# Optimization experiments

Measured on AMD Instinct MI355X. Metric: run time of the kernel, lower is better.

## Reference

```python
import jax, jax.numpy as jnp
import numpy as np

N, K = 50000, 16          # nodes, fixed neighbor-list length
IN, HID, OUT = 11, 64, 1  # temporal feat dim, hidden, output


def setup_inputs() -> dict:
    key = jax.random.key(0)
    ks = iter(jax.random.split(key, 64))
    def rn(shape, scale=1.0):
        return jax.random.normal(next(ks), shape, dtype=jnp.float32) * scale
    inp = {
        "x": rn((N, IN)),
        "neighbors": jax.random.randint(next(ks), (N, K), 0, N, dtype=jnp.int32),
        "prev_hidden": rn((N, HID)),
    }
    # DGL SAGEConv(lstm): LSTM(in=d, hid=d), fc_self Linear(d,o,bias=True), fc_neigh Linear(d,o,bias=False)
    dims = [(IN, HID), (HID, HID), (HID, HID), (HID, OUT)]
    for li, (d, o) in enumerate(dims, start=1):
        s = 1.0 / np.sqrt(d)
        inp[f"l{li}_Wih"] = rn((4 * d, d), s)
        inp[f"l{li}_Whh"] = rn((4 * d, d), s)
        inp[f"l{li}_bih"] = rn((4 * d,), s)
        inp[f"l{li}_bhh"] = rn((4 * d,), s)
        inp[f"l{li}_Ws"] = rn((o, d), s)
        inp[f"l{li}_bs"] = rn((o,), s)
        inp[f"l{li}_Wn"] = rn((o, d), s)
    sg = 1.0 / np.sqrt(HID)
    inp["g_Wih"] = rn((3 * HID, HID), sg)
    inp["g_Whh"] = rn((3 * HID, HID), sg)
    inp["g_bih"] = rn((3 * HID,), sg)
    inp["g_bhh"] = rn((3 * HID,), sg)
    return inp


def _sage_conv(h, neighbors, Wih, Whh, bih, bhh, Ws, bs, Wn):
    """DGL SAGEConv with aggregator_type='lstm'."""
    m = h[neighbors]             # [N, K, D] gathered neighbor messages
    ms = jnp.swapaxes(m, 0, 1)   # [K, N, D] time-major for scan
    Nn, D = h.shape
    h0 = jnp.zeros((Nn, D), h.dtype)

    def step(carry, mt):
        hp, cp = carry
        g = mt @ Wih.T + bih + hp @ Whh.T + bhh   # [N, 4D]
        i, f, gg, o = jnp.split(g, 4, axis=-1)    # torch LSTM gate order i,f,g,o
        c = jax.nn.sigmoid(f) * cp + jax.nn.sigmoid(i) * jnp.tanh(gg)
        hn = jax.nn.sigmoid(o) * jnp.tanh(c)
        return (hn, c), None

    (hK, _), _ = jax.lax.scan(step, (h0, h0), ms)  # final hidden state = neighbor agg
    return h @ Ws.T + bs + hK @ Wn.T


def _gru(x, h, Wih, Whh, bih, bhh):
    """torch.nn.GRUCell, gate order r,z,n."""
    gi = x @ Wih.T + bih
    gh = h @ Whh.T + bhh
    ir, iz, inn = jnp.split(gi, 3, axis=-1)
    hr, hz, hn = jnp.split(gh, 3, axis=-1)
    r = jax.nn.sigmoid(ir + hr)
    z = jax.nn.sigmoid(iz + hz)
    n = jnp.tanh(inn + r * hn)
    return (1.0 - z) * n + z * h


def reference(x, neighbors, prev_hidden,
              l1_Wih, l1_Whh, l1_bih, l1_bhh, l1_Ws, l1_bs, l1_Wn,
              l2_Wih, l2_Whh, l2_bih, l2_bhh, l2_Ws, l2_bs, l2_Wn,
              l3_Wih, l3_Whh, l3_bih, l3_bhh, l3_Ws, l3_bs, l3_Wn,
              l4_Wih, l4_Whh, l4_bih, l4_bhh, l4_Ws, l4_bs, l4_Wn,
              g_Wih, g_Whh, g_bih, g_bhh):
    h = jax.nn.relu(_sage_conv(x, neighbors, l1_Wih, l1_Whh, l1_bih, l1_bhh, l1_Ws, l1_bs, l1_Wn))
    h = jax.nn.relu(_sage_conv(h, neighbors, l2_Wih, l2_Whh, l2_bih, l2_bhh, l2_Ws, l2_bs, l2_Wn))
    h = jax.nn.relu(_sage_conv(h, neighbors, l3_Wih, l3_Whh, l3_bih, l3_bhh, l3_Ws, l3_bs, l3_Wn))
    h = _gru(h, prev_hidden, g_Wih, g_Whh, g_bih, g_bhh)
    logits = _sage_conv(h, neighbors, l4_Wih, l4_Whh, l4_bih, l4_bhh, l4_Ws, l4_bs, l4_Wn)
    return logits
```

## Files before the change

kernel.cpp:

```cpp
#include <hip/hip_runtime.h>

#define N_NODES 50000

typedef __bf16 bf16x8 __attribute__((ext_vector_type(8)));
typedef float f32x4 __attribute__((ext_vector_type(4)));

union U16x8 { uint4 v; unsigned short u[8]; bf16x8 b; };

__device__ __forceinline__ float b2f(unsigned short h){
  unsigned int u = ((unsigned int)h) << 16;
  return __builtin_bit_cast(float, u);
}
__device__ __forceinline__ unsigned short f2b(float x){
  unsigned int u = __builtin_bit_cast(unsigned int, x);
  u = u + 0x7FFFu + ((u >> 16) & 1u);
  return (unsigned short)(u >> 16);
}
__device__ __forceinline__ float sigm(float x){
  const float e = __builtin_amdgcn_exp2f(x * -1.4426950408889634f);
  return __builtin_amdgcn_rcpf(1.0f + e);
}
__device__ __forceinline__ float tanh_(float x){
  const float e = __builtin_amdgcn_exp2f(x * 2.8853900817779268f);
  return fmaf(-2.0f, __builtin_amdgcn_rcpf(1.0f + e), 1.0f);
}

__device__ __forceinline__ bf16x8 load8_bf16(const float* p){
  float4 a = *(const float4*)p; float4 c = *(const float4*)(p + 4);
  U16x8 r;
  r.u[0]=f2b(a.x); r.u[1]=f2b(a.y); r.u[2]=f2b(a.z); r.u[3]=f2b(a.w);
  r.u[4]=f2b(c.x); r.u[5]=f2b(c.y); r.u[6]=f2b(c.z); r.u[7]=f2b(c.w);
  return r.b;
}


__global__ __launch_bounds__(256) void l1_kernel(
    const float* __restrict__ x, const int* __restrict__ nbr,
    const float* __restrict__ Wih, const float* __restrict__ Whh,
    const float* __restrict__ bih, const float* __restrict__ bhh,
    const float* __restrict__ Ws,  const float* __restrict__ bs,
    const float* __restrict__ Wn,  unsigned short* __restrict__ out_hl)
{
  __shared__ unsigned short mbuf[16][16][24];
  __shared__ unsigned short hbuf[2][16][24];

  const int tid  = threadIdx.x;
  const int wave = tid >> 6, lane = tid & 63;
  const int n16  = lane & 15, q = lane >> 4;
  const int nb0  = blockIdx.x * 16;

  { unsigned int* p = (unsigned int*)hbuf;
    for (int i = tid; i < 384; i += 256) p[i] = 0u; }

  {
    const int nd = tid >> 4, t = tid & 15;
    const int gn = nbr[(nb0 + nd) * 16 + t];
    const float* row = x + (long)gn * 11;
    float v[16];
    #pragma unroll
    for (int j = 0; j < 11; j++) v[j] = row[j];
    #pragma unroll
    for (int j = 11; j < 16; j++) v[j] = 0.f;
    U16x8 A, B;
    #pragma unroll
    for (int j = 0; j < 8; j++){ A.u[j] = f2b(v[j]); B.u[j] = f2b(v[8 + j]); }
    *(uint4*)&mbuf[t][nd][0] = A.v;
    *(uint4*)&mbuf[t][nd][8] = B.v;
  }

  bf16x8 wf[4];
  float bg4[4];
  #pragma unroll
  for (int g = 0; g < 4; g++){
    const int u = n16;
    const float* src = (q < 2) ? (Wih + (g * 11 + u) * 11)
                               : (Whh + (g * 11 + u) * 11);
    const int kb = (q & 1) * 8;
    U16x8 a;
    #pragma unroll
    for (int j = 0; j < 8; j++){
      const int k = kb + j;
      float v = (u < 11 && k < 11) ? src[k] : 0.f;
      a.u[j] = f2b(v);
    }
    wf[g] = a.b;
    bg4[g] = (n16 < 11) ? (bih[g * 11 + n16] + bhh[g * 11 + n16]) : 0.f;
  }

  float c_ = 0.f;
  __syncthreads();

  for (int t = 0; t < 16; t++){
    const int db = t & 1, nb = db ^ 1;

    const unsigned short* ph = (q < 2) ? &mbuf[t][n16][q * 8]
                                       : &hbuf[db][n16][(q - 2) * 8];
    U16x8 ah; ah.v = *(const uint4*)ph;

    f32x4 acc[4];
    #pragma unroll
    for (int g = 0; g < 4; g++){
      f32x4 av = {bg4[g], bg4[g], bg4[g], bg4[g]};
      acc[g] = __builtin_amdgcn_mfma_f32_16x16x32_bf16(ah.b, wf[g], av, 0, 0, 0);
    }

    {
      const float iv = sigm(acc[0][wave]);
      const float fv = sigm(acc[1][wave]);
      const float gg = tanh_(acc[2][wave]);
      const float ov = sigm(acc[3][wave]);
      c_ = fv * c_ + iv * gg;
      hbuf[nb][q * 4 + wave][n16] = f2b(ov * tanh_(c_));
    }
    __syncthreads();
  }

  U16x8 ea;
  if (q < 2){
    const float* row = x + (long)(nb0 + n16) * 11;
    U16x8 H;
    #pragma unroll
    for (int j = 0; j < 8; j++){
      const int k = q * 8 + j;
      H.u[j] = f2b((k < 11) ? row[k] : 0.f);
    }
    ea = H;
  } else {
    ea.v = *(const uint4*)&hbuf[0][n16][(q - 2) * 8];
  }

  bf16x8 ewf;
  {
    const int uo = wave * 16 + n16;
    const float* src = (q < 2) ? (Ws + uo * 11) : (Wn + uo * 11);
    const int kb = (q & 1) * 8;
    U16x8 a;
    #pragma unroll
    for (int j = 0; j < 8; j++){
      const int k = kb + j;
      a.u[j] = f2b((k < 11) ? src[k] : 0.f);
    }
    ewf = a.b;
  }

  {
    const int uo = wave * 16 + n16;
    const float bsv = bs[uo];
    f32x4 e = {bsv, bsv, bsv, bsv};
    e = __builtin_amdgcn_mfma_f32_16x16x32_bf16(ea.b, ewf, e, 0, 0, 0);
    #pragma unroll
    for (int r = 0; r < 4; r++)
      out_hl[(size_t)(nb0 + q * 4 + r) * 64 + uo] = f2b(fmaxf(e[r], 0.f));
  }
}

__global__ __launch_bounds__(256, 3) void sage64_kernel(
    const unsigned short* __restrict__ in_hl, const int* __restrict__ nbr,
    const float* __restrict__ Wih, const float* __restrict__ Whh,
    const float* __restrict__ bih, const float* __restrict__ bhh,
    const float* __restrict__ Ws,  const float* __restrict__ bs,
    const float* __restrict__ Wn,
    unsigned short* __restrict__ out_hl, float* __restrict__ out_f32, int mode)
{
  __shared__ uint4 mbuf[8][16][8];
  __shared__ uint4 hbuf[2][16][8];

  const int tid = threadIdx.x;
  const int wv = tid >> 6, lane = tid & 63;
  const int n16 = lane & 15, q = lane >> 4;
  const int nb0 = blockIdx.x * 16;

  auto refill = [&](int base){
    const int nd = tid >> 4, sub = tid & 15;
    const int tr = sub >> 1, half = sub & 1;
    const int t_ = base + tr;
    const int gn = nbr[(nb0 + nd) * 16 + t_];
    const uint4* src = (const uint4*)(in_hl + (size_t)gn * 64);
    #pragma unroll
    for (int j = 0; j < 4; j++){
      const int s = half * 4 + j;
      mbuf[tr][nd][(s + nd + t_) & 7] = src[s];
    }
  };

  refill(0);
  { unsigned int* p = (unsigned int*)&hbuf[0][0][0];
    for (int i = tid; i < 512; i += 256) p[i] = 0u; }

  bf16x8 wih_f[4][2], whh_f[4][2];
  #pragma unroll
  for (int g = 0; g < 4; g++){
    const int row = g * 64 + wv * 16 + n16;
    #pragma unroll
    for (int kc = 0; kc < 2; kc++){
      wih_f[g][kc] = load8_bf16(Wih + row * 64 + kc * 32 + q * 8);
      whh_f[g][kc] = load8_bf16(Whh + row * 64 + kc * 32 + q * 8);
    }
  }
  f32x4 bg[4];
  #pragma unroll
  for (int g = 0; g < 4; g++){
    float4 bi = *(const float4*)(bih + g * 64 + wv * 16 + q * 4);
    float4 bh = *(const float4*)(bhh + g * 64 + wv * 16 + q * 4);
    f32x4 s = {bi.x + bh.x, bi.y + bh.y, bi.z + bh.z, bi.w + bh.w};
    bg[g] = s;
  }

  float c4[4] = {0.f, 0.f, 0.f, 0.f};
  __syncthreads();

  for (int t = 0; t < 16; t++){
    if (t == 8){
      refill(8);
      __syncthreads();
    }
    const int db = t & 1, nbf = db ^ 1;

    bf16x8 mh[2], hh[2];
    #pragma unroll
    for (int kc = 0; kc < 2; kc++){
      U16x8 a; a.v = mbuf[t & 7][n16][(kc * 4 + q + n16 + t) & 7]; mh[kc] = a.b;
      U16x8 c_; c_.v = hbuf[db][n16][(kc * 4 + q + n16) & 7];      hh[kc] = c_.b;
    }

    f32x4 acc[4];
    #pragma unroll
    for (int g = 0; g < 4; g++) acc[g] = bg[g];
    #pragma unroll
    for (int kc = 0; kc < 2; kc++){
      #pragma unroll
      for (int g = 0; g < 4; g++)
        acc[g] = __builtin_amdgcn_mfma_f32_16x16x32_bf16(wih_f[g][kc], mh[kc], acc[g], 0, 0, 0);
      #pragma unroll
      for (int g = 0; g < 4; g++)
        acc[g] = __builtin_amdgcn_mfma_f32_16x16x32_bf16(whh_f[g][kc], hh[kc], acc[g], 0, 0, 0);
    }

    unsigned short hB[4];
    #pragma unroll
    for (int r = 0; r < 4; r++){
      const float iv = sigm(acc[0][r]);
      const float fv = sigm(acc[1][r]);
      const float gg = tanh_(acc[2][r]);
      const float ov = sigm(acc[3][r]);
      c4[r] = fv * c4[r] + iv * gg;
      hB[r] = f2b(ov * tanh_(c4[r]));
    }
    {
      const int idx = wv * 4 + q;
      const int slot = idx >> 1, half = idx & 1;
      ((uint2*)&hbuf[nbf][n16][(slot + n16) & 7])[half] =
          make_uint2((unsigned)hB[0] | ((unsigned)hB[1] << 16),
                     (unsigned)hB[2] | ((unsigned)hB[3] << 16));
    }
    __syncthreads();
  }

  bf16x8 sH[2], kH[2];
  #pragma unroll
  for (int kc = 0; kc < 2; kc++){
    U16x8 a; a.v = *(const uint4*)(in_hl + (size_t)(nb0 + n16) * 64 + kc * 32 + q * 8);
    sH[kc] = a.b;
    U16x8 c_; c_.v = hbuf[0][n16][(kc * 4 + q + n16) & 7]; kH[kc] = c_.b;
  }

  if (mode == 0){
    bf16x8 ws_f[2], wn_f[2];
    #pragma unroll
    for (int kc = 0; kc < 2; kc++){
      ws_f[kc] = load8_bf16(Ws + (wv * 16 + n16) * 64 + kc * 32 + q * 8);
      wn_f[kc] = load8_bf16(Wn + (wv * 16 + n16) * 64 + kc * 32 + q * 8);
    }
    float4 bsv = *(const float4*)(bs + wv * 16 + q * 4);
    f32x4 e = {bsv.x, bsv.y, bsv.z, bsv.w};
    #pragma unroll
    for (int kc = 0; kc < 2; kc++){
      e = __builtin_amdgcn_mfma_f32_16x16x32_bf16(ws_f[kc], sH[kc], e, 0, 0, 0);
      e = __builtin_amdgcn_mfma_f32_16x16x32_bf16(wn_f[kc], kH[kc], e, 0, 0, 0);
    }
    unsigned short oB[4];
    #pragma unroll
    for (int r = 0; r < 4; r++) oB[r] = f2b(fmaxf(e[r], 0.f));
    *(uint2*)(out_hl + (size_t)(nb0 + n16) * 64 + wv * 16 + q * 4) =
        make_uint2((unsigned)oB[0] | ((unsigned)oB[1] << 16),
                   (unsigned)oB[2] | ((unsigned)oB[3] << 16));
  } else {
    if (wv == 0){
      bf16x8 ws_f[2], wn_f[2];
      #pragma unroll
      for (int kc = 0; kc < 2; kc++){
        U16x8 a, b_;
        a.v = make_uint4(0u,0u,0u,0u); b_.v = make_uint4(0u,0u,0u,0u);
        if (n16 == 0){
          a.b  = load8_bf16(Ws + kc * 32 + q * 8);
          b_.b = load8_bf16(Wn + kc * 32 + q * 8);
        }
        ws_f[kc] = a.b; wn_f[kc] = b_.b;
      }
      f32x4 e = {0.f, 0.f, 0.f, 0.f};
      #pragma unroll
      for (int kc = 0; kc < 2; kc++){
        e = __builtin_amdgcn_mfma_f32_16x16x32_bf16(ws_f[kc], sH[kc], e, 0, 0, 0);
        e = __builtin_amdgcn_mfma_f32_16x16x32_bf16(wn_f[kc], kH[kc], e, 0, 0, 0);
      }
      if (q == 0) out_f32[nb0 + n16] = e[0] + bs[0];
    }
  }
}

__global__ __launch_bounds__(256) void gru_kernel(
    const unsigned short* __restrict__ h3_hl, const float* __restrict__ prev,
    const float* __restrict__ gWih, const float* __restrict__ gWhh,
    const float* __restrict__ gbih, const float* __restrict__ gbhh,
    unsigned short* __restrict__ out_hl)
{
  const int tid = threadIdx.x, wave = tid >> 6, lane = tid & 63;
  const int n16 = lane & 15, q = lane >> 4;
  const int nb0 = blockIdx.x * 16;
  const int u_ = wave * 16 + n16;

  bf16x8 ah[2], ap[2];
  #pragma unroll
  for (int kc = 0; kc < 2; kc++){
    U16x8 a; a.v = *(const uint4*)(h3_hl + (size_t)(nb0 + n16) * 64 + kc * 32 + q * 8);
    ah[kc] = a.b;
    ap[kc] = load8_bf16(prev + (size_t)(nb0 + n16) * 64 + kc * 32 + q * 8);
  }

  bf16x8 wi_f[3][2], wh_f[3][2];
  #pragma unroll
  for (int g = 0; g < 3; g++){
    const int row = g * 64 + wave * 16 + n16;
    #pragma unroll
    for (int kc = 0; kc < 2; kc++){
      wi_f[g][kc] = load8_bf16(gWih + row * 64 + kc * 32 + q * 8);
      wh_f[g][kc] = load8_bf16(gWhh + row * 64 + kc * 32 + q * 8);
    }
  }

  f32x4 gi[3], gh[3];
  #pragma unroll
  for (int g = 0; g < 3; g++){
    const float bi = gbih[g * 64 + u_], bh = gbhh[g * 64 + u_];
    f32x4 vi = {bi, bi, bi, bi}; gi[g] = vi;
    f32x4 vh = {bh, bh, bh, bh}; gh[g] = vh;
  }
  #pragma unroll
  for (int kc = 0; kc < 2; kc++){
    #pragma unroll
    for (int g = 0; g < 3; g++)
      gi[g] = __builtin_amdgcn_mfma_f32_16x16x32_bf16(ah[kc], wi_f[g][kc], gi[g], 0, 0, 0);
    #pragma unroll
    for (int g = 0; g < 3; g++)
      gh[g] = __builtin_amdgcn_mfma_f32_16x16x32_bf16(ap[kc], wh_f[g][kc], gh[g], 0, 0, 0);
  }

  #pragma unroll
  for (int r = 0; r < 4; r++){
    const long node = nb0 + q * 4 + r;
    const float rv = sigm(gi[0][r] + gh[0][r]);
    const float zv = sigm(gi[1][r] + gh[1][r]);
    const float nv = tanh_(gi[2][r] + rv * gh[2][r]);
    const float hp = prev[node * 64 + u_];
    const float v = (1.f - zv) * nv + zv * hp;
    out_hl[(size_t)node * 64 + u_] = f2b(v);
  }
}

extern "C" void kernel_launch(void* const* d_in, const int* in_sizes, int n_in,
                              void* d_out, int out_size, void* d_ws, size_t ws_size,
                              hipStream_t stream)
{
  (void)in_sizes; (void)n_in; (void)out_size; (void)ws_size;
  const float* x    = (const float*)d_in[0];
  const int*   nbr  = (const int*)d_in[1];
  const float* prev = (const float*)d_in[2];
  auto W = [&](int i){ return (const float*)d_in[i]; };

  unsigned short* tabA = (unsigned short*)d_ws;
  unsigned short* tabB = tabA + (size_t)N_NODES * 64;

  l1_kernel<<<N_NODES / 16, 256, 0, stream>>>(
      x, nbr, W(3), W(4), W(5), W(6), W(7), W(8), W(9), tabA);
  sage64_kernel<<<N_NODES / 16, 256, 0, stream>>>(
      tabA, nbr, W(10), W(11), W(12), W(13), W(14), W(15), W(16), tabB, nullptr, 0);
  sage64_kernel<<<N_NODES / 16, 256, 0, stream>>>(
      tabB, nbr, W(17), W(18), W(19), W(20), W(21), W(22), W(23), tabA, nullptr, 0);
  gru_kernel<<<N_NODES / 16, 256, 0, stream>>>(
      tabA, prev, W(31), W(32), W(33), W(34), tabB);
  sage64_kernel<<<N_NODES / 16, 256, 0, stream>>>(
      tabB, nbr, W(24), W(25), W(26), W(27), W(28), W(29), W(30),
      nullptr, (float*)d_out, 1);
}
```

Measured before the change: 532.8 us.

## Process two 16-node groups per block in sage64 LSTM kernel

Each sage64 block now handles 32 nodes as two independent 16-node groups. Per-wave weight fragments in registers and the per-step barriers are shared across both groups, and the interleaved MFMA chains of the two groups give independent work to hide MFMA latency. In exchange the kernel uses twice the LDS and more registers, which may lower occupancy under the existing launch bounds, and the grid is halved, with guards for a partial last block.

```diff
diff --git a/kernel.cpp b/kernel.cpp
--- a/kernel.cpp
+++ b/kernel.cpp
@@ -162,30 +162,35 @@
     const float* __restrict__ Wn,
     unsigned short* __restrict__ out_hl, float* __restrict__ out_f32, int mode)
 {
-  __shared__ uint4 mbuf[8][16][8];
-  __shared__ uint4 hbuf[2][16][8];
+  __shared__ uint4 mbuf[2][8][16][8];
+  __shared__ uint4 hbuf[2][2][16][8];
 
   const int tid = threadIdx.x;
   const int wv = tid >> 6, lane = tid & 63;
   const int n16 = lane & 15, q = lane >> 4;
-  const int nb0 = blockIdx.x * 16;
-
-  auto refill = [&](int base){
+  const int nb0 = blockIdx.x * 32;
+  const int nb1 = nb0 + 16;
+  const bool v1 = (nb1 < N_NODES);
+
+  auto refill = [&](int grp, int base){
     const int nd = tid >> 4, sub = tid & 15;
     const int tr = sub >> 1, half = sub & 1;
     const int t_ = base + tr;
-    const int gn = nbr[(nb0 + nd) * 16 + t_];
+    int node = (grp ? nb1 : nb0) + nd;
+    if (node >= N_NODES) node = 0;
+    const int gn = nbr[node * 16 + t_];
     const uint4* src = (const uint4*)(in_hl + (size_t)gn * 64);
     #pragma unroll
     for (int j = 0; j < 4; j++){
       const int s = half * 4 + j;
-      mbuf[tr][nd][(s + nd + t_) & 7] = src[s];
+      mbuf[grp][tr][nd][(s + nd + t_) & 7] = src[s];
     }
   };
 
-  refill(0);
-  { unsigned int* p = (unsigned int*)&hbuf[0][0][0];
-    for (int i = tid; i < 512; i += 256) p[i] = 0u; }
+  refill(0, 0);
+  refill(1, 0);
+  { unsigned int* p = (unsigned int*)hbuf;
+    for (int i = tid; i < 2048; i += 256) p[i] = 0u; }
 
   bf16x8 wih_f[4][2], whh_f[4][2];
   #pragma unroll
@@ -206,62 +211,78 @@
     bg[g] = s;
   }
 
-  float c4[4] = {0.f, 0.f, 0.f, 0.f};
+  float c4[2][4] = {{0.f,0.f,0.f,0.f},{0.f,0.f,0.f,0.f}};
   __syncthreads();
 
   for (int t = 0; t < 16; t++){
     if (t == 8){
-      refill(8);
+      refill(0, 8);
+      refill(1, 8);
       __syncthreads();
     }
     const int db = t & 1, nbf = db ^ 1;
 
-    bf16x8 mh[2], hh[2];
+    bf16x8 mh[2][2], hh[2][2];
+    #pragma unroll
+    for (int grp = 0; grp < 2; grp++){
+      #pragma unroll
+      for (int kc = 0; kc < 2; kc++){
+        U16x8 a; a.v = mbuf[grp][t & 7][n16][(kc * 4 + q + n16 + t) & 7]; mh[grp][kc] = a.b;
+        U16x8 c_; c_.v = hbuf[grp][db][n16][(kc * 4 + q + n16) & 7];      hh[grp][kc] = c_.b;
+      }
+    }
+
+    f32x4 acc[2][4];
+    #pragma unroll
+    for (int grp = 0; grp < 2; grp++)
+      #pragma unroll
+      for (int g = 0; g < 4; g++) acc[grp][g] = bg[g];
     #pragma unroll
     for (int kc = 0; kc < 2; kc++){
-      U16x8 a; a.v = mbuf[t & 7][n16][(kc * 4 + q + n16 + t) & 7]; mh[kc] = a.b;
-      U16x8 c_; c_.v = hbuf[db][n16][(kc * 4 + q + n16) & 7];      hh[kc] = c_.b;
-    }
-
-    f32x4 acc[4];
-    #pragma unroll
-    for (int g = 0; g < 4; g++) acc[g] = bg[g];
-    #pragma unroll
-    for (int kc = 0; kc < 2; kc++){
-      #pragma unroll
-      for (int g = 0; g < 4; g++)
-        acc[g] = __builtin_amdgcn_mfma_f32_16x16x32_bf16(wih_f[g][kc], mh[kc], acc[g], 0, 0, 0);
-      #pragma unroll
-      for (int g = 0; g < 4; g++)
-        acc[g] = __builtin_amdgcn_mfma_f32_16x16x32_bf16(whh_f[g][kc], hh[kc], acc[g], 0, 0, 0);
-    }
-
-    unsigned short hB[4];
-    #pragma unroll
-    for (int r = 0; r < 4; r++){
-      const float iv = sigm(acc[0][r]);
-      const float fv = sigm(acc[1][r]);
-      const float gg = tanh_(acc[2][r]);
-      const float ov = sigm(acc[3][r]);
-      c4[r] = fv * c4[r] + iv * gg;
-      hB[r] = f2b(ov * tanh_(c4[r]));
-    }
-    {
+      #pragma unroll
+      for (int g = 0; g < 4; g++){
+        acc[0][g] = __builtin_amdgcn_mfma_f32_16x16x32_bf16(wih_f[g][kc], mh[0][kc], acc[0][g], 0, 0, 0);
+        acc[1][g] = __builtin_amdgcn_mfma_f32_16x16x32_bf16(wih_f[g][kc], mh[1][kc], acc[1][g], 0, 0, 0);
+      }
+      #pragma unroll
+      for (int g = 0; g < 4; g++){
+        acc[0][g] = __builtin_amdgcn_mfma_f32_16x16x32_bf16(whh_f[g][kc], hh[0][kc], acc[0][g], 0, 0, 0);
+        acc[1][g] = __builtin_amdgcn_mfma_f32_16x16x32_bf16(whh_f[g][kc], hh[1][kc], acc[1][g], 0, 0, 0);
+      }
+    }
+
+    #pragma unroll
+    for (int grp = 0; grp < 2; grp++){
+      unsigned short hB[4];
+      #pragma unroll
+      for (int r = 0; r < 4; r++){
+        const float iv = sigm(acc[grp][0][r]);
+        const float fv = sigm(acc[grp][1][r]);
+        const float gg = tanh_(acc[grp][2][r]);
+        const float ov = sigm(acc[grp][3][r]);
+        c4[grp][r] = fv * c4[grp][r] + iv * gg;
+        hB[r] = f2b(ov * tanh_(c4[grp][r]));
+      }
       const int idx = wv * 4 + q;
       const int slot = idx >> 1, half = idx & 1;
-      ((uint2*)&hbuf[nbf][n16][(slot + n16) & 7])[half] =
+      ((uint2*)&hbuf[grp][nbf][n16][(slot + n16) & 7])[half] =
           make_uint2((unsigned)hB[0] | ((unsigned)hB[1] << 16),
                      (unsigned)hB[2] | ((unsigned)hB[3] << 16));
     }
     __syncthreads();
   }
 
-  bf16x8 sH[2], kH[2];
-  #pragma unroll
-  for (int kc = 0; kc < 2; kc++){
-    U16x8 a; a.v = *(const uint4*)(in_hl + (size_t)(nb0 + n16) * 64 + kc * 32 + q * 8);
-    sH[kc] = a.b;
-    U16x8 c_; c_.v = hbuf[0][n16][(kc * 4 + q + n16) & 7]; kH[kc] = c_.b;
+  bf16x8 sH[2][2], kH[2][2];
+  #pragma unroll
+  for (int grp = 0; grp < 2; grp++){
+    int node = (grp ? nb1 : nb0) + n16;
+    if (node >= N_NODES) node = 0;
+    #pragma unroll
+    for (int kc = 0; kc < 2; kc++){
+      U16x8 a; a.v = *(const uint4*)(in_hl + (size_t)node * 64 + kc * 32 + q * 8);
+      sH[grp][kc] = a.b;
+      U16x8 c_; c_.v = hbuf[grp][0][n16][(kc * 4 + q + n16) & 7]; kH[grp][kc] = c_.b;
+    }
   }
 
   if (mode == 0){
@@ -272,20 +293,25 @@
       wn_f[kc] = load8_bf16(Wn + (wv * 16 + n16) * 64 + kc * 32 + q * 8);
     }
     float4 bsv = *(const float4*)(bs + wv * 16 + q * 4);
-    f32x4 e = {bsv.x, bsv.y, bsv.z, bsv.w};
-    #pragma unroll
-    for (int kc = 0; kc < 2; kc++){
-      e = __builtin_amdgcn_mfma_f32_16x16x32_bf16(ws_f[kc], sH[kc], e, 0, 0, 0);
-      e = __builtin_amdgcn_mfma_f32_16x16x32_bf16(wn_f[kc], kH[kc], e, 0, 0, 0);
-    }
-    unsigned short oB[4];
-    #pragma unroll
-    for (int r = 0; r < 4; r++) oB[r] = f2b(fmaxf(e[r], 0.f));
-    *(uint2*)(out_hl + (size_t)(nb0 + n16) * 64 + wv * 16 + q * 4) =
-        make_uint2((unsigned)oB[0] | ((unsigned)oB[1] << 16),
-                   (unsigned)oB[2] | ((unsigned)oB[3] << 16));
+    #pragma unroll
+    for (int grp = 0; grp < 2; grp++){
+      if (grp == 1 && !v1) break;
+      f32x4 e = {bsv.x, bsv.y, bsv.z, bsv.w};
+      #pragma unroll
+      for (int kc = 0; kc < 2; kc++){
+        e = __builtin_amdgcn_mfma_f32_16x16x32_bf16(ws_f[kc], sH[grp][kc], e, 0, 0, 0);
+        e = __builtin_amdgcn_mfma_f32_16x16x32_bf16(wn_f[kc], kH[grp][kc], e, 0, 0, 0);
+      }
+      unsigned short oB[4];
+      #pragma unroll
+      for (int r = 0; r < 4; r++) oB[r] = f2b(fmaxf(e[r], 0.f));
+      *(uint2*)(out_hl + (size_t)((grp ? nb1 : nb0) + n16) * 64 + wv * 16 + q * 4) =
+          make_uint2((unsigned)oB[0] | ((unsigned)oB[1] << 16),
+                     (unsigned)oB[2] | ((unsigned)oB[3] << 16));
+    }
   } else {
-    if (wv == 0){
+    if (wv < 2 && !(wv == 1 && !v1)){
+      const int grp = wv;
       bf16x8 ws_f[2], wn_f[2];
       #pragma unroll
       for (int kc = 0; kc < 2; kc++){
@@ -300,10 +326,10 @@
       f32x4 e = {0.f, 0.f, 0.f, 0.f};
       #pragma unroll
       for (int kc = 0; kc < 2; kc++){
-        e = __builtin_amdgcn_mfma_f32_16x16x32_bf16(ws_f[kc], sH[kc], e, 0, 0, 0);
-        e = __builtin_amdgcn_mfma_f32_16x16x32_bf16(wn_f[kc], kH[kc], e, 0, 0, 0);
-      }
-      if (q == 0) out_f32[nb0 + n16] = e[0] + bs[0];
+        e = __builtin_amdgcn_mfma_f32_16x16x32_bf16(ws_f[kc], sH[grp][kc], e, 0, 0, 0);
+        e = __builtin_amdgcn_mfma_f32_16x16x32_bf16(wn_f[kc], kH[grp][kc], e, 0, 0, 0);
+      }
+      if (q == 0) out_f32[(grp ? nb1 : nb0) + n16] = e[0] + bs[0];
     }
   }
 }
@@ -380,15 +406,17 @@
   unsigned short* tabA = (unsigned short*)d_ws;
   unsigned short* tabB = tabA + (size_t)N_NODES * 64;
 
+  const int sage_grid = (N_NODES + 31) / 32;
+
   l1_kernel<<<N_NODES / 16, 256, 0, stream>>>(
       x, nbr, W(3), W(4), W(5), W(6), W(7), W(8), W(9), tabA);
-  sage64_kernel<<<N_NODES / 16, 256, 0, stream>>>(
+  sage64_kernel<<<sage_grid, 256, 0, stream>>>(
       tabA, nbr, W(10), W(11), W(12), W(13), W(14), W(15), W(16), tabB, nullptr, 0);
-  sage64_kernel<<<N_NODES / 16, 256, 0, stream>>>(
+  sage64_kernel<<<sage_grid, 256, 0, stream>>>(
       tabB, nbr, W(17), W(18), W(19), W(20), W(21), W(22), W(23), tabA, nullptr, 0);
   gru_kernel<<<N_NODES / 16, 256, 0, stream>>>(
       tabA, prev, W(31), W(32), W(33), W(34), tabB);
-  sage64_kernel<<<N_NODES / 16, 256, 0, stream>>>(
+  sage64_kernel<<<sage_grid, 256, 0, stream>>>(
       tabB, nbr, W(24), W(25), W(26), W(27), W(28), W(29), W(30),
       nullptr, (float*)d_out, 1);
 }
```

After: 547.8 us. 1.03x slower.

## Fuse GRU cell into layer-3 SAGE kernel and prefetch all 16 neighbor steps

Applied to the files above, without the earlier changes.

The GRU cell now runs in the epilogue of the third SAGE layer: the layer-3 output tile goes into shared memory and the GRU matmuls are done in the same block. This drops a kernel launch and one global write and read of the intermediate activations. Separately, the neighbor-message buffer is doubled so all 16 timesteps are gathered up front, which removes the mid-loop refill and its barrier. The price is double the shared memory for mbuf (32KB) and more register pressure, which may reduce occupancy under launch_bounds(256,3).

```diff
diff --git a/kernel.cpp b/kernel.cpp
--- a/kernel.cpp
+++ b/kernel.cpp
@@ -160,9 +160,12 @@
     const float* __restrict__ bih, const float* __restrict__ bhh,
     const float* __restrict__ Ws,  const float* __restrict__ bs,
     const float* __restrict__ Wn,
+    const float* __restrict__ gWih, const float* __restrict__ gWhh,
+    const float* __restrict__ gbih, const float* __restrict__ gbhh,
+    const float* __restrict__ prevp,
     unsigned short* __restrict__ out_hl, float* __restrict__ out_f32, int mode)
 {
-  __shared__ uint4 mbuf[8][16][8];
+  __shared__ uint4 mbuf[16][16][8];
   __shared__ uint4 hbuf[2][16][8];
 
   const int tid = threadIdx.x;
@@ -170,20 +173,14 @@
   const int n16 = lane & 15, q = lane >> 4;
   const int nb0 = blockIdx.x * 16;
 
-  auto refill = [&](int base){
-    const int nd = tid >> 4, sub = tid & 15;
-    const int tr = sub >> 1, half = sub & 1;
-    const int t_ = base + tr;
-    const int gn = nbr[(nb0 + nd) * 16 + t_];
+  {
+    const int nd = tid >> 4, t = tid & 15;
+    const int gn = nbr[(nb0 + nd) * 16 + t];
     const uint4* src = (const uint4*)(in_hl + (size_t)gn * 64);
     #pragma unroll
-    for (int j = 0; j < 4; j++){
-      const int s = half * 4 + j;
-      mbuf[tr][nd][(s + nd + t_) & 7] = src[s];
-    }
-  };
-
-  refill(0);
+    for (int s = 0; s < 8; s++)
+      mbuf[t][nd][(s + nd + t) & 7] = src[s];
+  }
   { unsigned int* p = (unsigned int*)&hbuf[0][0][0];
     for (int i = tid; i < 512; i += 256) p[i] = 0u; }
 
@@ -210,17 +207,13 @@
   __syncthreads();
 
   for (int t = 0; t < 16; t++){
-    if (t == 8){
-      refill(8);
-      __syncthreads();
-    }
     const int db = t & 1, nbf = db ^ 1;
 
     bf16x8 mh[2], hh[2];
     #pragma unroll
     for (int kc = 0; kc < 2; kc++){
-      U16x8 a; a.v = mbuf[t & 7][n16][(kc * 4 + q + n16 + t) & 7]; mh[kc] = a.b;
-      U16x8 c_; c_.v = hbuf[db][n16][(kc * 4 + q + n16) & 7];      hh[kc] = c_.b;
+      U16x8 a; a.v = mbuf[t][n16][(kc * 4 + q + n16 + t) & 7];  mh[kc] = a.b;
+      U16x8 c_; c_.v = hbuf[db][n16][(kc * 4 + q + n16) & 7];   hh[kc] = c_.b;
     }
 
     f32x4 acc[4];
@@ -264,7 +257,7 @@
     U16x8 c_; c_.v = hbuf[0][n16][(kc * 4 + q + n16) & 7]; kH[kc] = c_.b;
   }
 
-  if (mode == 0){
+  if (mode != 1){
     bf16x8 ws_f[2], wn_f[2];
     #pragma unroll
     for (int kc = 0; kc < 2; kc++){
@@ -281,9 +274,66 @@
     unsigned short oB[4];
     #pragma unroll
     for (int r = 0; r < 4; r++) oB[r] = f2b(fmaxf(e[r], 0.f));
-    *(uint2*)(out_hl + (size_t)(nb0 + n16) * 64 + wv * 16 + q * 4) =
-        make_uint2((unsigned)oB[0] | ((unsigned)oB[1] << 16),
-                   (unsigned)oB[2] | ((unsigned)oB[3] << 16));
+    const uint2 packed = make_uint2((unsigned)oB[0] | ((unsigned)oB[1] << 16),
+                                    (unsigned)oB[2] | ((unsigned)oB[3] << 16));
+
+    if (mode == 0){
+      *(uint2*)(out_hl + (size_t)(nb0 + n16) * 64 + wv * 16 + q * 4) = packed;
+    } else {
+      {
+        const int idx = wv * 4 + q;
+        const int slot = idx >> 1, half = idx & 1;
+        ((uint2*)&hbuf[1][n16][(slot + n16) & 7])[half] = packed;
+      }
+      __syncthreads();
+
+      bf16x8 x3[2], pv[2];
+      #pragma unroll
+      for (int kc = 0; kc < 2; kc++){
+        U16x8 a; a.v = hbuf[1][n16][(kc * 4 + q + n16) & 7]; x3[kc] = a.b;
+        pv[kc] = load8_bf16(prevp + (size_t)(nb0 + n16) * 64 + kc * 32 + q * 8);
+      }
+      bf16x8 wi_f[3][2], wh_f[3][2];
+      #pragma unroll
+      for (int g = 0; g < 3; g++){
+        const int row = g * 64 + wv * 16 + n16;
+        #pragma unroll
+        for (int kc = 0; kc < 2; kc++){
+          wi_f[g][kc] = load8_bf16(gWih + row * 64 + kc * 32 + q * 8);
+          wh_f[g][kc] = load8_bf16(gWhh + row * 64 + kc * 32 + q * 8);
+        }
+      }
+      f32x4 gi[3], gh[3];
+      #pragma unroll
+      for (int g = 0; g < 3; g++){
+        float4 bi = *(const float4*)(gbih + g * 64 + wv * 16 + q * 4);
+        float4 bh = *(const float4*)(gbhh + g * 64 + wv * 16 + q * 4);
+        f32x4 vi = {bi.x, bi.y, bi.z, bi.w}; gi[g] = vi;
+        f32x4 vh = {bh.x, bh.y, bh.z, bh.w}; gh[g] = vh;
+      }
+      #pragma unroll
+      for (int kc = 0; kc < 2; kc++){
+        #pragma unroll
+        for (int g = 0; g < 3; g++)
+          gi[g] = __builtin_amdgcn_mfma_f32_16x16x32_bf16(wi_f[g][kc], x3[kc], gi[g], 0, 0, 0);
+        #pragma unroll
+        for (int g = 0; g < 3; g++)
+          gh[g] = __builtin_amdgcn_mfma_f32_16x16x32_bf16(wh_f[g][kc], pv[kc], gh[g], 0, 0, 0);
+      }
+      float4 hp4 = *(const float4*)(prevp + (size_t)(nb0 + n16) * 64 + wv * 16 + q * 4);
+      const float hp[4] = {hp4.x, hp4.y, hp4.z, hp4.w};
+      unsigned short gB[4];
+      #pragma unroll
+      for (int r = 0; r < 4; r++){
+        const float rv = sigm(gi[0][r] + gh[0][r]);
+        const float zv = sigm(gi[1][r] + gh[1][r]);
+        const float nv = tanh_(gi[2][r] + rv * gh[2][r]);
+        gB[r] = f2b((1.f - zv) * nv + zv * hp[r]);
+      }
+      *(uint2*)(out_hl + (size_t)(nb0 + n16) * 64 + wv * 16 + q * 4) =
+          make_uint2((unsigned)gB[0] | ((unsigned)gB[1] << 16),
+                     (unsigned)gB[2] | ((unsigned)gB[3] << 16));
+    }
   } else {
     if (wv == 0){
       bf16x8 ws_f[2], wn_f[2];
@@ -305,65 +355,6 @@
       }
       if (q == 0) out_f32[nb0 + n16] = e[0] + bs[0];
     }
-  }
-}
-
-__global__ __launch_bounds__(256) void gru_kernel(
-    const unsigned short* __restrict__ h3_hl, const float* __restrict__ prev,
-    const float* __restrict__ gWih, const float* __restrict__ gWhh,
-    const float* __restrict__ gbih, const float* __restrict__ gbhh,
-    unsigned short* __restrict__ out_hl)
-{
-  const int tid = threadIdx.x, wave = tid >> 6, lane = tid & 63;
-  const int n16 = lane & 15, q = lane >> 4;
-  const int nb0 = blockIdx.x * 16;
-  const int u_ = wave * 16 + n16;
-
-  bf16x8 ah[2], ap[2];
-  #pragma unroll
-  for (int kc = 0; kc < 2; kc++){
-    U16x8 a; a.v = *(const uint4*)(h3_hl + (size_t)(nb0 + n16) * 64 + kc * 32 + q * 8);
-    ah[kc] = a.b;
-    ap[kc] = load8_bf16(prev + (size_t)(nb0 + n16) * 64 + kc * 32 + q * 8);
-  }
-
-  bf16x8 wi_f[3][2], wh_f[3][2];
-  #pragma unroll
-  for (int g = 0; g < 3; g++){
-    const int row = g * 64 + wave * 16 + n16;
-    #pragma unroll
-    for (int kc = 0; kc < 2; kc++){
-      wi_f[g][kc] = load8_bf16(gWih + row * 64 + kc * 32 + q * 8);
-      wh_f[g][kc] = load8_bf16(gWhh + row * 64 + kc * 32 + q * 8);
-    }
-  }
-
-  f32x4 gi[3], gh[3];
-  #pragma unroll
-  for (int g = 0; g < 3; g++){
-    const float bi = gbih[g * 64 + u_], bh = gbhh[g * 64 + u_];
-    f32x4 vi = {bi, bi, bi, bi}; gi[g] = vi;
-    f32x4 vh = {bh, bh, bh, bh}; gh[g] = vh;
-  }
-  #pragma unroll
-  for (int kc = 0; kc < 2; kc++){
-    #pragma unroll
-    for (int g = 0; g < 3; g++)
-      gi[g] = __builtin_amdgcn_mfma_f32_16x16x32_bf16(ah[kc], wi_f[g][kc], gi[g], 0, 0, 0);
-    #pragma unroll
-    for (int g = 0; g < 3; g++)
-      gh[g] = __builtin_amdgcn_mfma_f32_16x16x32_bf16(ap[kc], wh_f[g][kc], gh[g], 0, 0, 0);
-  }
-
-  #pragma unroll
-  for (int r = 0; r < 4; r++){
-    const long node = nb0 + q * 4 + r;
-    const float rv = sigm(gi[0][r] + gh[0][r]);
-    const float zv = sigm(gi[1][r] + gh[1][r]);
-    const float nv = tanh_(gi[2][r] + rv * gh[2][r]);
-    const float hp = prev[node * 64 + u_];
-    const float v = (1.f - zv) * nv + zv * hp;
-    out_hl[(size_t)node * 64 + u_] = f2b(v);
   }
 }
 
@@ -383,12 +374,15 @@
   l1_kernel<<<N_NODES / 16, 256, 0, stream>>>(
       x, nbr, W(3), W(4), W(5), W(6), W(7), W(8), W(9), tabA);
   sage64_kernel<<<N_NODES / 16, 256, 0, stream>>>(
-      tabA, nbr, W(10), W(11), W(12), W(13), W(14), W(15), W(16), tabB, nullptr, 0);
+      tabA, nbr, W(10), W(11), W(12), W(13), W(14), W(15), W(16),
+      nullptr, nullptr, nullptr, nullptr, nullptr,
+      tabB, nullptr, 0);
   sage64_kernel<<<N_NODES / 16, 256, 0, stream>>>(
-      tabB, nbr, W(17), W(18), W(19), W(20), W(21), W(22), W(23), tabA, nullptr, 0);
-  gru_kernel<<<N_NODES / 16, 256, 0, stream>>>(
-      tabA, prev, W(31), W(32), W(33), W(34), tabB);
+      tabB, nbr, W(17), W(18), W(19), W(20), W(21), W(22), W(23),
+      W(31), W(32), W(33), W(34), prev,
+      tabA, nullptr, 2);
   sage64_kernel<<<N_NODES / 16, 256, 0, stream>>>(
-      tabB, nbr, W(24), W(25), W(26), W(27), W(28), W(29), W(30),
+      tabA, nbr, W(24), W(25), W(26), W(27), W(28), W(29), W(30),
+      nullptr, nullptr, nullptr, nullptr, nullptr,
       nullptr, (float*)d_out, 1);
 }
```

Result: faster. 484.9 us (-9.0%).
